# Kernel tuning notes

Hardware: AMD Instinct MI355X
Metric: run time of the kernel (lower is better)

The kernel has to match this reference:

```python
import jax, jax.numpy as jnp
import numpy as np


def setup_inputs() -> dict:
    key = jax.random.key(0)
    k1, k2 = jax.random.split(key)
    WS, M, K, N = 8, 8192, 512, 1024  # world_size, tokens, local-K, N
    inp = jax.random.normal(k1, (WS, M, K), dtype=jnp.float32)
    weight = jax.random.normal(k2, (WS, N, K), dtype=jnp.float32) * 0.02
    return {"input": inp, "weight": weight}


def reference(input, weight):
    # Per-rank partial GEMM: input [ws, M, K] x weight [ws, N, K] -> [ws, M, N]
    ws, M, _ = input.shape
    N = weight.shape[1]
    Ms = M // ws  # rows per rank after reduce-scatter
    partial = jnp.einsum("wmk,wnk->wmn", input, weight)
    # Reduce-scatter over M dim: rank r receives sum over ranks of rows [r*Ms:(r+1)*Ms]
    # partial -> [src_rank=ws, dst_rank=ws, Ms, N], sum over src_rank
    out = partial.reshape(ws, ws, Ms, N).sum(axis=0)  # [ws, Ms, N]
    return out
```

## Files before the change

### kernel.cpp

```cpp
#include <hip/hip_runtime.h>
#include <hip/hip_bf16.h>


#define WS 8
#define MM 8192
#define KK 512
#define NN 1024
#define KTOT (WS * KK)
#define BM 128
#define BN 64
#define BK 64
#define ITERS (KTOT / BK)

#define A_ELEMS ((size_t)WS * MM * KK)
#define B_ELEMS ((size_t)WS * NN * KK)
#define WS_NEEDED ((A_ELEMS + B_ELEMS) * 2)

typedef __attribute__((ext_vector_type(8))) short short8;
typedef __attribute__((ext_vector_type(4))) short short4v;
typedef __attribute__((ext_vector_type(4))) float floatx4;

static __device__ inline short f2bf(float f) {
    union { __hip_bfloat16 h; short s; } u;
    u.h = __float2bfloat16(f);
    return u.s;
}

static __device__ inline void glds16(const short* g, short* l) {
    __builtin_amdgcn_global_load_lds(
        (const __attribute__((address_space(1))) unsigned int*)(uintptr_t)g,
        (__attribute__((address_space(3))) unsigned int*)(uintptr_t)l,
        16, 0, 0);
}

#define CVT_ABLOCKS 16384
#define CVT_NBLOCKS 18432

__global__ __launch_bounds__(256)
void cvt_f32_bf16(const float* __restrict__ A, const float* __restrict__ B,
                  short* __restrict__ Abf, short* __restrict__ Bbf) {
    const float* src;
    short* dst;
    size_t base;
    if (blockIdx.x < CVT_ABLOCKS) {
        src = A; dst = Abf;
        base = ((size_t)blockIdx.x * 256 + threadIdx.x) * 8;
    } else {
        src = B; dst = Bbf;
        base = ((size_t)(blockIdx.x - CVT_ABLOCKS) * 256 + threadIdx.x) * 8;
    }
    float4 v0 = *(const float4*)(src + base);
    float4 v1 = *(const float4*)(src + base + 4);
    short8 o = { f2bf(v0.x), f2bf(v0.y), f2bf(v0.z), f2bf(v0.w),
                 f2bf(v1.x), f2bf(v1.y), f2bf(v1.z), f2bf(v1.w) };
    *(short8*)(dst + base) = o;
}

__global__ __launch_bounds__(256, 3)
void gemm_bf16_rs(const short* __restrict__ Abf, const short* __restrict__ Bbf,
                  float* __restrict__ C) {
    __shared__ short As[2][BM * BK];
    __shared__ short Bs[2][BN * BK];

    const int tid  = threadIdx.x;
    const int lane = tid & 63;
    const int wid  = tid >> 6;
    const int m0 = blockIdx.y * BM;
    const int n0 = blockIdx.x * BN;
    const int wr = wid >> 1, wc = wid & 1;
    const int lm = lane & 15, quad = lane >> 4;

    const int lrow = lane >> 3;
    const int ss   = (lane & 7) ^ lrow;

    size_t gA[4], gB[2];
#pragma unroll
    for (int t = 0; t < 4; ++t)
        gA[t] = (size_t)(m0 + wid * 32 + t * 8 + lrow) * KK + ss * 8;
#pragma unroll
    for (int t = 0; t < 2; ++t)
        gB[t] = (size_t)(n0 + wid * 16 + t * 8 + lrow) * KK + ss * 8;

    floatx4 acc[4][2];
#pragma unroll
    for (int i = 0; i < 4; ++i)
#pragma unroll
        for (int j = 0; j < 2; ++j) acc[i][j] = (floatx4)0.f;

#pragma unroll
    for (int q = 0; q < 4; ++q)
        glds16(Abf + gA[q], &As[0][(wid * 4 + q) * 512 + lane * 8]);
#pragma unroll
    for (int q = 0; q < 2; ++q)
        glds16(Bbf + gB[q], &Bs[0][(wid * 2 + q) * 512 + lane * 8]);

    for (int t = 0; t < ITERS; ++t) {
        const int p  = t & 1;
        const int tn = (t + 1) & (ITERS - 1);
        const int np = tn & 1;
        const int wn = tn >> 3;
        const int kn = (tn & 7) * BK;
        const short* Aw = Abf + (size_t)wn * MM * KK + kn;
        const short* Bw = Bbf + (size_t)wn * NN * KK + kn;

#pragma unroll
        for (int q = 0; q < 4; ++q)
            glds16(Aw + gA[q], &As[np][(wid * 4 + q) * 512 + lane * 8]);
#pragma unroll
        for (int q = 0; q < 2; ++q)
            glds16(Bw + gB[q], &Bs[np][(wid * 2 + q) * 512 + lane * 8]);

        asm volatile("s_waitcnt vmcnt(6)" ::: "memory");
        asm volatile("s_barrier" ::: "memory");

        short8 af[2][4], bfr[2][2];
#pragma unroll
        for (int kc = 0; kc < 2; ++kc) {
#pragma unroll
            for (int i = 0; i < 4; ++i) {
                const int row = wr * 64 + i * 16 + lm;
                const int sa  = (kc * 4 + quad) ^ (lm & 7);
                af[kc][i] = *(const short8*)&As[p][row * BK + sa * 8];
            }
#pragma unroll
            for (int j = 0; j < 2; ++j) {
                const int row = wc * 32 + j * 16 + lm;
                const int sb  = (kc * 4 + quad) ^ (lm & 7);
                bfr[kc][j] = *(const short8*)&Bs[p][row * BK + sb * 8];
            }
        }
#pragma unroll
        for (int kc = 0; kc < 2; ++kc)
#pragma unroll
            for (int i = 0; i < 4; ++i)
#pragma unroll
                for (int j = 0; j < 2; ++j)
                    acc[i][j] = __builtin_amdgcn_mfma_f32_16x16x32_bf16(
                        af[kc][i], bfr[kc][j], acc[i][j], 0, 0, 0);

        asm volatile("s_barrier" ::: "memory");
    }

#pragma unroll
    for (int i = 0; i < 4; ++i)
#pragma unroll
        for (int j = 0; j < 2; ++j) {
            const int n = n0 + wc * 32 + j * 16 + lm;
#pragma unroll
            for (int r = 0; r < 4; ++r) {
                const int m = m0 + wr * 64 + i * 16 + quad * 4 + r;
                C[(size_t)m * NN + n] = acc[i][j][r];
            }
        }
}

__global__ __launch_bounds__(256, 2)
void gemm_rs_fused(const float* __restrict__ A, const float* __restrict__ B,
                   float* __restrict__ C) {
    __shared__ short As[128 * 32];
    __shared__ short Bs[128 * 32];
    const int tid = threadIdx.x;
    const int m0 = blockIdx.y * 128;
    const int n0 = blockIdx.x * 128;
    const int wid = tid >> 6, lane = tid & 63;
    const int wr = wid >> 1, wc = wid & 1;
    const int lm = lane & 15, quad = lane >> 4;
    floatx4 acc[4][4];
#pragma unroll
    for (int i = 0; i < 4; ++i)
#pragma unroll
        for (int j = 0; j < 4; ++j) acc[i][j] = (floatx4)0.f;
    for (int kt = 0; kt < KTOT; kt += 32) {
        const int w = kt >> 9, kk = kt & (KK - 1);
        const float* Aw = A + (size_t)w * MM * KK;
        const float* Bw = B + (size_t)w * NN * KK;
        __syncthreads();
#pragma unroll
        for (int i = 0; i < 4; ++i) {
            const int idx = i * 256 + tid;
            const int row = idx >> 3;
            const int c4 = (idx & 7) * 4;
            float4 av = *(const float4*)&Aw[(size_t)(m0 + row) * KK + kk + c4];
            float4 bv = *(const float4*)&Bw[(size_t)(n0 + row) * KK + kk + c4];
            short4v a4 = { f2bf(av.x), f2bf(av.y), f2bf(av.z), f2bf(av.w) };
            short4v b4 = { f2bf(bv.x), f2bf(bv.y), f2bf(bv.z), f2bf(bv.w) };
            *(short4v*)&As[row * 32 + c4] = a4;
            *(short4v*)&Bs[row * 32 + c4] = b4;
        }
        __syncthreads();
        short8 af[4], bfr[4];
#pragma unroll
        for (int i = 0; i < 4; ++i)
            af[i] = *(const short8*)&As[(wr * 64 + i * 16 + lm) * 32 + quad * 8];
#pragma unroll
        for (int j = 0; j < 4; ++j)
            bfr[j] = *(const short8*)&Bs[(wc * 64 + j * 16 + lm) * 32 + quad * 8];
#pragma unroll
        for (int i = 0; i < 4; ++i)
#pragma unroll
            for (int j = 0; j < 4; ++j)
                acc[i][j] = __builtin_amdgcn_mfma_f32_16x16x32_bf16(
                    af[i], bfr[j], acc[i][j], 0, 0, 0);
    }
#pragma unroll
    for (int i = 0; i < 4; ++i)
#pragma unroll
        for (int j = 0; j < 4; ++j) {
            const int n = n0 + wc * 64 + j * 16 + lm;
#pragma unroll
            for (int r = 0; r < 4; ++r) {
                const int m = m0 + wr * 64 + i * 16 + quad * 4 + r;
                C[(size_t)m * NN + n] = acc[i][j][r];
            }
        }
}

extern "C" void kernel_launch(void* const* d_in, const int* in_sizes, int n_in,
                              void* d_out, int out_size, void* d_ws, size_t ws_size,
                              hipStream_t stream) {
    const float* A = (const float*)d_in[0];
    const float* B = (const float*)d_in[1];
    float* C = (float*)d_out;

    if (ws_size >= WS_NEEDED) {
        short* Abf = (short*)d_ws;
        short* Bbf = Abf + A_ELEMS;
        cvt_f32_bf16<<<CVT_NBLOCKS, 256, 0, stream>>>(A, B, Abf, Bbf);
        dim3 grid(NN / BN, MM / BM);
        gemm_bf16_rs<<<grid, 256, 0, stream>>>(Abf, Bbf, C);
    } else {
        dim3 grid(NN / 128, MM / 128);
        gemm_rs_fused<<<grid, 256, 0, stream>>>(A, B, C);
    }
}
```

Measured before the change: 301.8 us.

## Use 256x128 tiles with 32x32x16 MFMA and register-resident B fragments

Grows the GEMM block tile from 128x64 to 256x128 and switches the 16x16x32 MFMA for the 32x32x16 bf16 instruction, so each wave computes a 128x64 sub-tile. B fragments are now loaded straight from global memory into double-buffered registers instead of going through LDS, and only A is staged in LDS. The grid is also swapped so blockIdx.x walks M. The aim is more operand reuse per load and less LDS traffic, at the cost of higher register pressure (occupancy drops to 1 block per CU), redundant global loads of B across waves, and a grid of only 256 blocks.

```diff
diff --git a/kernel.cpp b/kernel.cpp
--- a/kernel.cpp
+++ b/kernel.cpp
@@ -7,8 +7,8 @@
 #define KK 512
 #define NN 1024
 #define KTOT (WS * KK)
-#define BM 128
-#define BN 64
+#define BMt 256
+#define BNt 128
 #define BK 64
 #define ITERS (KTOT / BK)
 
@@ -19,6 +19,7 @@
 typedef __attribute__((ext_vector_type(8))) short short8;
 typedef __attribute__((ext_vector_type(4))) short short4v;
 typedef __attribute__((ext_vector_type(4))) float floatx4;
+typedef __attribute__((ext_vector_type(16))) float floatx16;
 
 static __device__ inline short f2bf(float f) {
     union { __hip_bfloat16 h; short s; } u;
@@ -56,43 +57,46 @@
     *(short8*)(dst + base) = o;
 }
 
-__global__ __launch_bounds__(256, 3)
+__global__ __launch_bounds__(256, 1)
 void gemm_bf16_rs(const short* __restrict__ Abf, const short* __restrict__ Bbf,
                   float* __restrict__ C) {
-    __shared__ short As[2][BM * BK];
-    __shared__ short Bs[2][BN * BK];
+    __shared__ short As[2][BMt * BK];
 
     const int tid  = threadIdx.x;
     const int lane = tid & 63;
     const int wid  = tid >> 6;
-    const int m0 = blockIdx.y * BM;
-    const int n0 = blockIdx.x * BN;
+    const int m0 = blockIdx.x * BMt;
+    const int n0 = blockIdx.y * BNt;
     const int wr = wid >> 1, wc = wid & 1;
-    const int lm = lane & 15, quad = lane >> 4;
+    const int l31   = lane & 31;
+    const int khalf = lane >> 5;
 
     const int lrow = lane >> 3;
     const int ss   = (lane & 7) ^ lrow;
-
-    size_t gA[4], gB[2];
-#pragma unroll
-    for (int t = 0; t < 4; ++t)
-        gA[t] = (size_t)(m0 + wid * 32 + t * 8 + lrow) * KK + ss * 8;
-#pragma unroll
-    for (int t = 0; t < 2; ++t)
-        gB[t] = (size_t)(n0 + wid * 16 + t * 8 + lrow) * KK + ss * 8;
-
-    floatx4 acc[4][2];
-#pragma unroll
-    for (int i = 0; i < 4; ++i)
-#pragma unroll
-        for (int j = 0; j < 2; ++j) acc[i][j] = (floatx4)0.f;
-
-#pragma unroll
-    for (int q = 0; q < 4; ++q)
-        glds16(Abf + gA[q], &As[0][(wid * 4 + q) * 512 + lane * 8]);
-#pragma unroll
-    for (int q = 0; q < 2; ++q)
-        glds16(Bbf + gB[q], &Bs[0][(wid * 2 + q) * 512 + lane * 8]);
+    size_t gA[8];
+#pragma unroll
+    for (int q = 0; q < 8; ++q)
+        gA[q] = (size_t)(m0 + wid * 64 + q * 8 + lrow) * KK + ss * 8;
+
+    const int nIdx = n0 + wc * 64 + l31;
+
+    floatx16 acc[4][2];
+#pragma unroll
+    for (int i = 0; i < 4; ++i)
+#pragma unroll
+        for (int j = 0; j < 2; ++j) acc[i][j] = (floatx16)0.f;
+
+    short8 breg[2][2][4];
+
+#pragma unroll
+    for (int j = 0; j < 2; ++j)
+#pragma unroll
+        for (int kc = 0; kc < 4; ++kc)
+            breg[0][j][kc] = *(const short8*)&Bbf[(size_t)(nIdx + j * 32) * KK +
+                                                  kc * 16 + khalf * 8];
+#pragma unroll
+    for (int q = 0; q < 8; ++q)
+        glds16(Abf + gA[q], &As[0][(wid * 8 + q) * 512 + lane * 8]);
 
     for (int t = 0; t < ITERS; ++t) {
         const int p  = t & 1;
@@ -104,39 +108,34 @@
         const short* Bw = Bbf + (size_t)wn * NN * KK + kn;
 
 #pragma unroll
-        for (int q = 0; q < 4; ++q)
-            glds16(Aw + gA[q], &As[np][(wid * 4 + q) * 512 + lane * 8]);
-#pragma unroll
-        for (int q = 0; q < 2; ++q)
-            glds16(Bw + gB[q], &Bs[np][(wid * 2 + q) * 512 + lane * 8]);
-
-        asm volatile("s_waitcnt vmcnt(6)" ::: "memory");
+        for (int j = 0; j < 2; ++j)
+#pragma unroll
+            for (int kc = 0; kc < 4; ++kc)
+                breg[np][j][kc] = *(const short8*)&Bw[(size_t)(nIdx + j * 32) * KK +
+                                                      kc * 16 + khalf * 8];
+#pragma unroll
+        for (int q = 0; q < 8; ++q)
+            glds16(Aw + gA[q], &As[np][(wid * 8 + q) * 512 + lane * 8]);
+
+        asm volatile("s_waitcnt vmcnt(16)" ::: "memory");
         asm volatile("s_barrier" ::: "memory");
 
-        short8 af[2][4], bfr[2][2];
-#pragma unroll
-        for (int kc = 0; kc < 2; ++kc) {
+#pragma unroll
+        for (int kc = 0; kc < 4; ++kc) {
+            short8 af[4];
 #pragma unroll
             for (int i = 0; i < 4; ++i) {
-                const int row = wr * 64 + i * 16 + lm;
-                const int sa  = (kc * 4 + quad) ^ (lm & 7);
-                af[kc][i] = *(const short8*)&As[p][row * BK + sa * 8];
+                const int row = wr * 128 + i * 32 + l31;
+                const int seg = (kc * 2 + khalf) ^ (lane & 7);
+                af[i] = *(const short8*)&As[p][row * BK + seg * 8];
             }
 #pragma unroll
-            for (int j = 0; j < 2; ++j) {
-                const int row = wc * 32 + j * 16 + lm;
-                const int sb  = (kc * 4 + quad) ^ (lm & 7);
-                bfr[kc][j] = *(const short8*)&Bs[p][row * BK + sb * 8];
-            }
-        }
-#pragma unroll
-        for (int kc = 0; kc < 2; ++kc)
-#pragma unroll
             for (int i = 0; i < 4; ++i)
 #pragma unroll
                 for (int j = 0; j < 2; ++j)
-                    acc[i][j] = __builtin_amdgcn_mfma_f32_16x16x32_bf16(
-                        af[kc][i], bfr[kc][j], acc[i][j], 0, 0, 0);
+                    acc[i][j] = __builtin_amdgcn_mfma_f32_32x32x16_bf16(
+                        af[i], breg[p][j][kc], acc[i][j], 0, 0, 0);
+        }
 
         asm volatile("s_barrier" ::: "memory");
     }
@@ -145,10 +144,11 @@
     for (int i = 0; i < 4; ++i)
 #pragma unroll
         for (int j = 0; j < 2; ++j) {
-            const int n = n0 + wc * 32 + j * 16 + lm;
-#pragma unroll
-            for (int r = 0; r < 4; ++r) {
-                const int m = m0 + wr * 64 + i * 16 + quad * 4 + r;
+            const int n = n0 + wc * 64 + j * 32 + l31;
+            const int mb = m0 + wr * 128 + i * 32 + 4 * khalf;
+#pragma unroll
+            for (int r = 0; r < 16; ++r) {
+                const int m = mb + (r & 3) + 8 * (r >> 2);
                 C[(size_t)m * NN + n] = acc[i][j][r];
             }
         }
@@ -157,8 +157,8 @@
 __global__ __launch_bounds__(256, 2)
 void gemm_rs_fused(const float* __restrict__ A, const float* __restrict__ B,
                    float* __restrict__ C) {
-    __shared__ short As[128 * 32];
-    __shared__ short Bs[128 * 32];
+    __shared__ short Asf[128 * 32];
+    __shared__ short Bsf[128 * 32];
     const int tid = threadIdx.x;
     const int m0 = blockIdx.y * 128;
     const int n0 = blockIdx.x * 128;
@@ -184,17 +184,17 @@
             float4 bv = *(const float4*)&Bw[(size_t)(n0 + row) * KK + kk + c4];
             short4v a4 = { f2bf(av.x), f2bf(av.y), f2bf(av.z), f2bf(av.w) };
             short4v b4 = { f2bf(bv.x), f2bf(bv.y), f2bf(bv.z), f2bf(bv.w) };
-            *(short4v*)&As[row * 32 + c4] = a4;
-            *(short4v*)&Bs[row * 32 + c4] = b4;
+            *(short4v*)&Asf[row * 32 + c4] = a4;
+            *(short4v*)&Bsf[row * 32 + c4] = b4;
         }
         __syncthreads();
         short8 af[4], bfr[4];
 #pragma unroll
         for (int i = 0; i < 4; ++i)
-            af[i] = *(const short8*)&As[(wr * 64 + i * 16 + lm) * 32 + quad * 8];
+            af[i] = *(const short8*)&Asf[(wr * 64 + i * 16 + lm) * 32 + quad * 8];
 #pragma unroll
         for (int j = 0; j < 4; ++j)
-            bfr[j] = *(const short8*)&Bs[(wc * 64 + j * 16 + lm) * 32 + quad * 8];
+            bfr[j] = *(const short8*)&Bsf[(wc * 64 + j * 16 + lm) * 32 + quad * 8];
 #pragma unroll
         for (int i = 0; i < 4; ++i)
 #pragma unroll
@@ -226,7 +226,7 @@
         short* Abf = (short*)d_ws;
         short* Bbf = Abf + A_ELEMS;
         cvt_f32_bf16<<<CVT_NBLOCKS, 256, 0, stream>>>(A, B, Abf, Bbf);
-        dim3 grid(NN / BN, MM / BM);
+        dim3 grid(MM / BMt, NN / BNt);
         gemm_bf16_rs<<<grid, 256, 0, stream>>>(Abf, Bbf, C);
     } else {
         dim3 grid(NN / 128, MM / 128);
```

Measured after the change: 439.6 us. 1.46x slower.
